# Performance work log

Hardware: AMD Instinct MI355X
Metric: run time of the kernel (lower is better)

## Reference

```python
import jax, jax.numpy as jnp
import numpy as np

B, C, IMG, P = 64, 3, 224, 16
D, L, H, DH, M, NC = 768, 12, 12, 64, 3072, 1000
INNER = H * DH
PD = C * P * P          # patch_dim = 768
NP = (IMG // P) ** 2    # 196 patches


def setup_inputs() -> dict:
    key = jax.random.key(0)
    ks = jax.random.split(key, 16)
    s = 0.02
    nrm = lambda k, shape: jax.random.normal(k, shape, jnp.float32) * s
    return dict(
        img=jax.random.normal(ks[0], (B, C, IMG, IMG), jnp.float32),
        patch_ln1_g=jnp.ones(PD), patch_ln1_b=jnp.zeros(PD),
        patch_w=nrm(ks[1], (PD, D)), patch_b=jnp.zeros(D),
        patch_ln2_g=jnp.ones(D), patch_ln2_b=jnp.zeros(D),
        pos_emb=nrm(ks[2], (1, NP + 1, D)),
        cls_tok=nrm(ks[3], (1, 1, D)),
        attn_ln_g=jnp.ones((L, D)), attn_ln_b=jnp.zeros((L, D)),
        w_qkv=nrm(ks[4], (L, D, 3 * INNER)),
        w_out=nrm(ks[5], (L, INNER, D)), b_out=jnp.zeros((L, D)),
        ff_ln_g=jnp.ones((L, D)), ff_ln_b=jnp.zeros((L, D)),
        ff_w1=nrm(ks[6], (L, D, M)), ff_b1=jnp.zeros((L, M)),
        ff_w2=nrm(ks[7], (L, M, D)), ff_b2=jnp.zeros((L, D)),
        final_ln_g=jnp.ones(D), final_ln_b=jnp.zeros(D),
        head_w=nrm(ks[8], (D, NC)), head_b=jnp.zeros(NC),
    )


def _ln(x, g, b, eps=1e-5):
    m = x.mean(-1, keepdims=True)
    v = ((x - m) ** 2).mean(-1, keepdims=True)
    return (x - m) / jnp.sqrt(v + eps) * g + b


def reference(img, patch_ln1_g, patch_ln1_b, patch_w, patch_b, patch_ln2_g,
              patch_ln2_b, pos_emb, cls_tok, attn_ln_g, attn_ln_b, w_qkv,
              w_out, b_out, ff_ln_g, ff_ln_b, ff_w1, ff_b1, ff_w2, ff_b2,
              final_ln_g, final_ln_b, head_w, head_b):
    b, c, hh, ww = img.shape
    h, w = hh // P, ww // P
    # Rearrange 'b c (h p1) (w p2) -> b (h w) (p1 p2 c)'
    x = img.reshape(b, c, h, P, w, P).transpose(0, 2, 4, 3, 5, 1).reshape(b, h * w, P * P * c)
    x = _ln(x, patch_ln1_g, patch_ln1_b)
    x = x @ patch_w + patch_b
    x = _ln(x, patch_ln2_g, patch_ln2_b)
    n = x.shape[1]
    x = jnp.concatenate([jnp.broadcast_to(cls_tok, (b, 1, x.shape[-1])), x], axis=1)
    x = x + pos_emb[:, : n + 1]
    scale = DH ** -0.5
    for l in range(L):
        xn = _ln(x, attn_ln_g[l], attn_ln_b[l])
        qkv = xn @ w_qkv[l]  # [b, n+1, 3*inner]
        q, k, v = jnp.split(qkv, 3, axis=-1)
        sp = lambda t: t.reshape(b, -1, H, DH).transpose(0, 2, 1, 3)  # b h n d
        q, k, v = sp(q), sp(k), sp(v)
        # softmax variant: exp(scores*scale), normalize by sum + eps (no max-subtract, faithful to source)
        numer = jnp.exp(jnp.einsum('bhid,bhjd->bhij', q, k) * scale)
        attn = numer / (numer.sum(-1, keepdims=True) + 1e-8)
        out = jnp.einsum('bhij,bhjd->bhid', attn, v)
        out = out.transpose(0, 2, 1, 3).reshape(b, -1, INNER)
        x = out @ w_out[l] + b_out[l] + x
        xn = _ln(x, ff_ln_g[l], ff_ln_b[l])
        hid = jax.nn.gelu(xn @ ff_w1[l] + ff_b1[l], approximate=False)
        x = hid @ ff_w2[l] + ff_b2[l] + x
    x = _ln(x, final_ln_g, final_ln_b)
    return x[:, 0] @ head_w + head_b
```

## Files before the change

### kernel.cpp

```cpp
#include <hip/hip_runtime.h>
#include <hip/hip_bf16.h>
#include <math.h>

#define B_     64
#define NTOK   197
#define NPATCH 196
#define D768   768
#define NL     12
#define NH     12
#define MFF    3072
#define NCLS   1000
#define ROWS   (B_ * NTOK)
#define PROWS  (B_ * NPATCH)
#define ROWS_PAD 12672

typedef unsigned short ushort;
typedef __bf16 bf16x8 __attribute__((ext_vector_type(8)));
typedef float  f32x4  __attribute__((ext_vector_type(4)));
typedef unsigned short u16x4 __attribute__((ext_vector_type(4)));

__device__ __forceinline__ ushort f2b(float f) {
  __hip_bfloat16 h = __float2bfloat16(f);
  return *reinterpret_cast<ushort*>(&h);
}
__device__ __forceinline__ float b2f(ushort u) {
  unsigned int v = ((unsigned int)u) << 16;
  float f;
  __builtin_memcpy(&f, &v, 4);
  return f;
}

__device__ __forceinline__ void gload16(const ushort* g, ushort* lds) {
  __builtin_amdgcn_global_load_lds((const __attribute__((address_space(1))) void*)g,
                                   (__attribute__((address_space(3))) void*)lds, 16, 0, 0);
}

__device__ __forceinline__ float gelu_f(float v) {
  float t = v * fmaf(0.0713548162726f, v * v, 1.5957691216f);
  return v / (1.0f + __expf(-t));
}

__device__ __forceinline__ void block_mean_rstd(float s, float sq, float& mean, float& rstd) {
#pragma unroll
  for (int off = 32; off; off >>= 1) { s += __shfl_xor(s, off); sq += __shfl_xor(sq, off); }
  __shared__ float ss[4], ssq[4];
  int w = threadIdx.x >> 6;
  if ((threadIdx.x & 63) == 0) { ss[w] = s; ssq[w] = sq; }
  __syncthreads();
  s  = ss[0] + ss[1] + ss[2] + ss[3];
  sq = ssq[0] + ssq[1] + ssq[2] + ssq[3];
  mean = s * (1.0f / 768.0f);
  float var = sq * (1.0f / 768.0f) - mean * mean;
  rstd = rsqrtf(var + 1e-5f);
}

__global__ __launch_bounds__(256) void ln_rows4(const ushort* __restrict__ in, long in_stride,
                                                const float* __restrict__ g,
                                                const float* __restrict__ bta,
                                                ushort* __restrict__ out) {
  const int w = threadIdx.x >> 6, l = threadIdx.x & 63;
  const size_t row = (size_t)blockIdx.x * 4 + w;
  const ushort* xr = in + row * in_stride;
  u16x4 xv[3];
  xv[0] = *(const u16x4*)(xr + l * 4);
  xv[1] = *(const u16x4*)(xr + 256 + l * 4);
  xv[2] = *(const u16x4*)(xr + 512 + l * 4);
  float v[12];
  float s = 0.f, sq = 0.f;
#pragma unroll
  for (int i = 0; i < 3; ++i)
#pragma unroll
    for (int j = 0; j < 4; ++j) {
      float f = b2f(xv[i][j]);
      v[i * 4 + j] = f;
      s += f; sq += f * f;
    }
#pragma unroll
  for (int off = 32; off; off >>= 1) { s += __shfl_xor(s, off); sq += __shfl_xor(sq, off); }
  float mean = s * (1.0f / 768.0f);
  float rstd = rsqrtf(sq * (1.0f / 768.0f) - mean * mean + 1e-5f);
  ushort* o = out + row * 768;
#pragma unroll
  for (int i = 0; i < 3; ++i) {
    int base = i * 256 + l * 4;
    f32x4 gv = *(const f32x4*)(g + base);
    f32x4 bv = *(const f32x4*)(bta + base);
    u16x4 ov = { f2b((v[i*4+0] - mean) * rstd * gv[0] + bv[0]),
                 f2b((v[i*4+1] - mean) * rstd * gv[1] + bv[1]),
                 f2b((v[i*4+2] - mean) * rstd * gv[2] + bv[2]),
                 f2b((v[i*4+3] - mean) * rstd * gv[3] + bv[3]) };
    *(u16x4*)(o + base) = ov;
  }
}

__global__ __launch_bounds__(256) void patch_ln1(const float* __restrict__ img,
                                                 const float* __restrict__ g,
                                                 const float* __restrict__ bta,
                                                 ushort* __restrict__ xp) {
  int pidx = blockIdx.x;
  int b = pidx / NPATCH, hw = pidx % NPATCH;
  int ph = hw / 14, pw = hw % 14;
  int t = threadIdx.x;
  int p1 = t >> 4, p2 = t & 15;
  float v[3];
#pragma unroll
  for (int c = 0; c < 3; ++c)
    v[c] = img[(((size_t)b * 3 + c) * 224 + ph * 16 + p1) * 224 + pw * 16 + p2];
  float mean, rstd;
  block_mean_rstd(v[0] + v[1] + v[2], v[0] * v[0] + v[1] * v[1] + v[2] * v[2], mean, rstd);
  ushort* o = xp + (size_t)pidx * 768;
#pragma unroll
  for (int c = 0; c < 3; ++c) {
    int k = t * 3 + c;
    o[k] = f2b((v[c] - mean) * rstd * g[k] + bta[k]);
  }
}

__global__ __launch_bounds__(256) void ln2_pos(const float* __restrict__ xe,
                                               const float* __restrict__ g,
                                               const float* __restrict__ bta,
                                               const float* __restrict__ pos,
                                               ushort* __restrict__ x) {
  int pidx = blockIdx.x;
  int b = pidx / NPATCH, i = pidx % NPATCH;
  const float* xr = xe + (size_t)pidx * 768;
  int t = threadIdx.x;
  float v0 = xr[t], v1 = xr[t + 256], v2 = xr[t + 512];
  float mean, rstd;
  block_mean_rstd(v0 + v1 + v2, v0 * v0 + v1 * v1 + v2 * v2, mean, rstd);
  const float* p = pos + (size_t)(1 + i) * 768;
  ushort* o = x + ((size_t)b * NTOK + 1 + i) * 768;
  o[t]       = f2b((v0 - mean) * rstd * g[t]       + bta[t]       + p[t]);
  o[t + 256] = f2b((v1 - mean) * rstd * g[t + 256] + bta[t + 256] + p[t + 256]);
  o[t + 512] = f2b((v2 - mean) * rstd * g[t + 512] + bta[t + 512] + p[t + 512]);
}

__global__ __launch_bounds__(256) void cls_init(const float* __restrict__ cls_tok,
                                                const float* __restrict__ pos,
                                                ushort* __restrict__ x) {
  int b = blockIdx.x, t = threadIdx.x;
  ushort* o = x + (size_t)b * NTOK * 768;
#pragma unroll
  for (int u = 0; u < 3; ++u) { int k = t + u * 256; o[k] = f2b(cls_tok[k] + pos[k]); }
}

__global__ __launch_bounds__(256) void transpose_cast(const float* __restrict__ W,
                                                      ushort* __restrict__ Wt,
                                                      int K, int N) {
  __shared__ float t[32][33];
  int n0 = blockIdx.x * 32, k0 = blockIdx.y * 32;
  int tx = threadIdx.x, ty = threadIdx.y;
#pragma unroll
  for (int u = 0; u < 32; u += 8) {
    int n = n0 + tx;
    t[ty + u][tx] = (n < N) ? W[(size_t)(k0 + ty + u) * N + n] : 0.f;
  }
  __syncthreads();
#pragma unroll
  for (int u = 0; u < 32; u += 8) {
    int n = n0 + ty + u;
    if (n < N) Wt[(size_t)n * K + k0 + tx] = f2b(t[tx][ty + u]);
  }
}

__device__ __forceinline__ void transpose_layer128(int bid,
                                                   const float* wq, const float* wo,
                                                   const float* w1, const float* w2,
                                                   ushort* tq, ushort* to,
                                                   ushort* t1, ushort* t2) {
  const float* W; ushort* Wt; int K, N, xt;
  if (bid < 216)      {             W = wq; Wt = tq; K = 768;  N = 2304; xt = 36; }
  else if (bid < 288) { bid -= 216; W = wo; Wt = to; K = 768;  N = 768;  xt = 12; }
  else if (bid < 576) { bid -= 288; W = w1; Wt = t1; K = 768;  N = 3072; xt = 48; }
  else                { bid -= 576; W = w2; Wt = t2; K = 3072; N = 768;  xt = 12; }
  int n0 = (bid % xt) * 64, k0 = (bid / xt) * 128;
  __shared__ float t[128 * 64];
  int id = threadIdx.x;
#pragma unroll
  for (int pass = 0; pass < 8; ++pass) {
    int c = pass * 256 + id;
    int k = c >> 4, col = (c & 15) * 4;
    f32x4 v = *(const f32x4*)(W + (size_t)(k0 + k) * N + n0 + col);
    int s = (k >> 2) & 31;
#pragma unroll
    for (int j = 0; j < 4; ++j) t[k * 64 + ((col + j) ^ s)] = v[j];
  }
  __syncthreads();
#pragma unroll
  for (int pass = 0; pass < 8; ++pass) {
    int c = pass * 256 + id;
    int n = c >> 5, k = (c & 31) * 4;
    int s = (k >> 2) & 31;
    u16x4 o = { f2b(t[(k + 0) * 64 + (n ^ s)]),
                f2b(t[(k + 1) * 64 + (n ^ s)]),
                f2b(t[(k + 2) * 64 + (n ^ s)]),
                f2b(t[(k + 3) * 64 + (n ^ s)]) };
    *(u16x4*)(Wt + (size_t)(n0 + n) * K + k0 + k) = o;
  }
}

__global__ __launch_bounds__(256) void transpose4(const float* __restrict__ wq,
                                                  const float* __restrict__ wo,
                                                  const float* __restrict__ w1,
                                                  const float* __restrict__ w2,
                                                  ushort* __restrict__ tq,
                                                  ushort* __restrict__ to,
                                                  ushort* __restrict__ t1,
                                                  ushort* __restrict__ t2) {
  transpose_layer128(blockIdx.x, wq, wo, w1, w2, tq, to, t1, t2);
}

__global__ __launch_bounds__(256) void transpose_all(const float* __restrict__ wq,
                                                     const float* __restrict__ wo,
                                                     const float* __restrict__ w1,
                                                     const float* __restrict__ w2,
                                                     ushort* __restrict__ tq,
                                                     ushort* __restrict__ to,
                                                     ushort* __restrict__ t1,
                                                     ushort* __restrict__ t2) {
  int l = blockIdx.x / 864, bid = blockIdx.x % 864;
  transpose_layer128(bid,
                     wq + (size_t)l * 768 * 2304, wo + (size_t)l * 768 * 768,
                     w1 + (size_t)l * 768 * MFF,  w2 + (size_t)l * MFF * 768,
                     tq + (size_t)l * 2304 * 768, to + (size_t)l * 768 * 768,
                     t1 + (size_t)l * MFF * 768,  t2 + (size_t)l * 768 * MFF);
}

template<int EP, int RESID, int OBF>
__global__ __launch_bounds__(256, 4) void gemm_v6(const ushort* __restrict__ A,
                                                  const ushort* __restrict__ Bt,
                                                  const float* __restrict__ bias,
                                                  const void* __restrict__ resid,
                                                  void* __restrict__ Cv,
                                                  int M, int N, int K) {
  __shared__ ushort smem[2 * 8192];

  const int tid = threadIdx.x;
  const int w = tid >> 6, l = tid & 63;
  const int fr = l & 15, fc = l >> 4;

  const int ntx = gridDim.x;
  const int nwg = ntx * gridDim.y;
  const int orig = blockIdx.y * ntx + blockIdx.x;
  const int q = nwg >> 3, r = nwg & 7, xcd = orig & 7, idx = orig >> 3;
  const int wg = (xcd < r ? xcd * (q + 1) : r * (q + 1) + (xcd - r) * q) + idx;
  const int row0 = (wg / ntx) * 128, col0 = (wg % ntx) * 128;

  const int wr = (w >> 1) * 64, wc = (w & 1) * 64;

  const int srow = tid >> 2;
  const int sg = (tid & 3) ^ ((srow >> 1) & 3);
  const ushort* pA0 = A  + (size_t)(row0 + srow) * K + sg * 8;
  const ushort* pA1 = A  + (size_t)(row0 + 64 + srow) * K + sg * 8;
  const ushort* pB0 = Bt + (size_t)(col0 + srow) * K + sg * 8;
  const ushort* pB1 = Bt + (size_t)(col0 + 64 + srow) * K + sg * 8;

  auto stage = [&](int t_, ushort* dst) {
    const int k0 = t_ * 32;
    gload16(pA0 + k0, dst + tid * 8);
    gload16(pA1 + k0, dst + (tid + 256) * 8);
    gload16(pB0 + k0, dst + 4096 + tid * 8);
    gload16(pB1 + k0, dst + 4096 + (tid + 256) * 8);
  };

  int idxA[4], idxB[4];
#pragma unroll
  for (int m = 0; m < 4; ++m) {
    int rA = wr + m * 16 + fr;
    idxA[m] = rA * 32 + ((fc ^ ((rA >> 1) & 3)) << 3);
  }
#pragma unroll
  for (int n = 0; n < 4; ++n) {
    int rB = wc + n * 16 + fr;
    idxB[n] = rB * 32 + ((fc ^ ((rB >> 1) & 3)) << 3);
  }

  f32x4 acc[4][4] = {};

  auto compute = [&](const ushort* As) {
    const ushort* Bs = As + 4096;
    bf16x8 a_[4], b_[4];
#pragma unroll
    for (int m = 0; m < 4; ++m) a_[m] = *(const bf16x8*)(As + idxA[m]);
#pragma unroll
    for (int n = 0; n < 4; ++n) b_[n] = *(const bf16x8*)(Bs + idxB[n]);
#pragma unroll
    for (int m = 0; m < 4; ++m)
#pragma unroll
      for (int n = 0; n < 4; ++n)
        acc[m][n] = __builtin_amdgcn_mfma_f32_16x16x32_bf16(b_[n], a_[m], acc[m][n], 0, 0, 0);
  };

#define VM4() asm volatile("s_waitcnt vmcnt(4)" ::: "memory")
#define VM0() asm volatile("s_waitcnt vmcnt(0)" ::: "memory")

  const int NT = K >> 5;

  stage(0, smem);
  for (int t = 0; t < NT; t += 2) {
    if (t + 1 < NT) { stage(t + 1, smem + 8192); VM4(); } else VM0();
    __builtin_amdgcn_s_barrier();
    compute(smem);
    __builtin_amdgcn_s_barrier();
    if (t + 1 < NT) {
      if (t + 2 < NT) { stage(t + 2, smem); VM4(); } else VM0();
      __builtin_amdgcn_s_barrier();
      compute(smem + 8192);
      __builtin_amdgcn_s_barrier();
    }
  }
#undef VM4
#undef VM0

  if (!OBF) {
    float* Cf = (float*)Cv;
#pragma unroll
    for (int m = 0; m < 4; ++m) {
      int row = row0 + wr + m * 16 + fr;
      if (row >= M) continue;
#pragma unroll
      for (int n = 0; n < 4; ++n) {
        int col = col0 + wc + n * 16 + fc * 4;
        f32x4 v = acc[m][n];
        if (bias) v += *(const f32x4*)(bias + col);
        if (EP) {
#pragma unroll
          for (int rr = 0; rr < 4; ++rr) v[rr] = gelu_f(v[rr]);
        }
        if (RESID) v += *(const f32x4*)((const float*)resid + (size_t)row * N + col);
        *(f32x4*)(Cf + (size_t)row * N + col) = v;
      }
    }
  } else {
    __syncthreads();
    ushort* Cw = smem + w * 4096;
#pragma unroll
    for (int m = 0; m < 4; ++m) {
      int rl = m * 16 + fr;
      int row = row0 + wr + rl;
#pragma unroll
      for (int n = 0; n < 4; ++n) {
        int col = col0 + wc + n * 16 + fc * 4;
        f32x4 v = acc[m][n];
        if (bias) v += *(const f32x4*)(bias + col);
        if (EP) {
#pragma unroll
          for (int rr = 0; rr < 4; ++rr) v[rr] = gelu_f(v[rr]);
        }
        if (RESID) {
          u16x4 rv = *(const u16x4*)((const ushort*)resid + (size_t)row * N + col);
#pragma unroll
          for (int rr = 0; rr < 4; ++rr) v[rr] += b2f(rv[rr]);
        }
        u16x4 pk = { f2b(v[0]), f2b(v[1]), f2b(v[2]), f2b(v[3]) };
        int s = (n * 4 + fc) ^ (rl & 7);
        *(u16x4*)(Cw + rl * 64 + s * 4) = pk;
      }
    }
    ushort* Cb = (ushort*)Cv;
#pragma unroll
    for (int pp = 0; pp < 16; ++pp) {
      int rl = pp * 4 + (l >> 4);
      int cs = l & 15;
      u16x4 pk = *(const u16x4*)(Cw + rl * 64 + ((cs ^ (rl & 7)) * 4));
      int row = row0 + wr + rl;
      if (row < M) *(u16x4*)(Cb + (size_t)row * N + col0 + wc + cs * 4) = pk;
    }
  }
}

template<int EP, int RESID, int OBF>
__global__ __launch_bounds__(256) void gemm_bt(const ushort* __restrict__ A,
                                               const ushort* __restrict__ Bt,
                                               const float* __restrict__ bias,
                                               const float* __restrict__ resid,
                                               void* __restrict__ C,
                                               int M, int N, int K) {
  __shared__ ushort As[128 * 32];
  __shared__ ushort Bs[128 * 32];
  int tid = threadIdx.x;
  int w = tid >> 6, l = tid & 63;
  int fr = l & 15, fc = l >> 4;
  int row0 = blockIdx.y * 128, col0 = blockIdx.x * 128;
  int wr = (w >> 1) * 64, wc = (w & 1) * 64;

  int srow0 = w * 32 + (l >> 2);
  int srow1 = srow0 + 16;
  int sc0 = (((l & 3) ^ ((srow0 >> 1) & 3)) << 3);
  int sc1 = (((l & 3) ^ ((srow1 >> 1) & 3)) << 3);
  const ushort* ga0 = A  + (size_t)(row0 + srow0) * K + sc0;
  const ushort* ga1 = A  + (size_t)(row0 + srow1) * K + sc1;
  const ushort* gb0 = Bt + (size_t)(col0 + srow0) * K + sc0;
  const ushort* gb1 = Bt + (size_t)(col0 + srow1) * K + sc1;

  int idxA[4], idxB[4];
#pragma unroll
  for (int m = 0; m < 4; ++m) {
    int rA = wr + m * 16 + fr;
    idxA[m] = rA * 32 + ((fc ^ ((rA >> 1) & 3)) << 3);
  }
#pragma unroll
  for (int n = 0; n < 4; ++n) {
    int rB = wc + n * 16 + fr;
    idxB[n] = rB * 32 + ((fc ^ ((rB >> 1) & 3)) << 3);
  }

  f32x4 acc[4][4] = {};

  for (int k0 = 0; k0 < K; k0 += 32) {
    gload16(ga0 + k0, &As[w * 1024]);
    gload16(ga1 + k0, &As[w * 1024 + 512]);
    gload16(gb0 + k0, &Bs[w * 1024]);
    gload16(gb1 + k0, &Bs[w * 1024 + 512]);
    __syncthreads();
    bf16x8 af[4], bfr[4];
#pragma unroll
    for (int m = 0; m < 4; ++m) af[m] = *(const bf16x8*)(As + idxA[m]);
#pragma unroll
    for (int n = 0; n < 4; ++n) bfr[n] = *(const bf16x8*)(Bs + idxB[n]);
#pragma unroll
    for (int m = 0; m < 4; ++m)
#pragma unroll
      for (int n = 0; n < 4; ++n)
        acc[m][n] = __builtin_amdgcn_mfma_f32_16x16x32_bf16(af[m], bfr[n], acc[m][n], 0, 0, 0);
    __syncthreads();
  }

#pragma unroll
  for (int n = 0; n < 4; ++n) {
    int col = col0 + wc + n * 16 + fr;
    if (col >= N) continue;
    float bv = bias ? bias[col] : 0.f;
#pragma unroll
    for (int m = 0; m < 4; ++m) {
#pragma unroll
      for (int rr = 0; rr < 4; ++rr) {
        int row = row0 + wr + m * 16 + fc * 4 + rr;
        if (row >= M) continue;
        float v = acc[m][n][rr] + bv;
        if (EP == 1) v = 0.5f * v * (1.0f + erff(v * 0.70710678118654752f));
        if (RESID) v += resid[(size_t)row * N + col];
        if (OBF) ((ushort*)C)[(size_t)row * N + col] = f2b(v);
        else     ((float*)C)[(size_t)row * N + col]  = v;
      }
    }
  }
}

__global__ __launch_bounds__(256) void attn_mfma(const ushort* __restrict__ qkv,
                                                 ushort* __restrict__ aout) {
  int bidp = blockIdx.x;
  int bh = (bidp & 7) | ((bidp >> 5) << 3);
  int qt = (bidp >> 3) & 3;
  int h  = bh % NH;
  int b  = bh / NH;
  int tid = threadIdx.x, w = tid >> 6, l = tid & 63;
  int fr = l & 15, fc = l >> 4;

  __shared__ ushort Kt[64 * 64];
  __shared__ ushort Vt[64 * 64];
  __shared__ ushort Pl[4 * 16 * 64];

  const size_t brow = (size_t)b * NTOK;
  int q0 = qt * 64 + w * 16;

  const int skey = tid >> 3;
  const int sgk = (tid & 7) ^ ((skey >> 1) & 7);
  const ushort* pK0 = qkv + (brow + skey) * 2304 + 768 + h * 64 + sgk * 8;
  const ushort* pK1 = qkv + (brow + 32 + skey) * 2304 + 768 + h * 64 + sgk * 8;

  bf16x8 qf[2];
  {
    const ushort* qp = qkv + (brow + q0 + fr) * 2304 + h * 64 + fc * 8;
    qf[0] = *(const bf16x8*)qp;
    qf[1] = *(const bf16x8*)(qp + 32);
  }
  float rs[4] = {0.f, 0.f, 0.f, 0.f};
  f32x4 oc[4] = {};

  for (int kt = 0; kt < 4; ++kt) {
    __syncthreads();
    {
      const size_t koff = (size_t)kt * 64 * 2304;
      gload16(pK0 + koff, Kt + tid * 8);
      gload16(pK1 + koff, Kt + (tid + 256) * 8);
    }
    {
      int key = tid >> 2, d0 = (tid & 3) * 16;
      int j = kt * 64 + key;
      bool valid = j < NTOK;
      const ushort* vp = qkv + (brow + j) * 2304 + 1536 + h * 64 + d0;
      ushort vbuf[16];
      if (valid) {
        *(bf16x8*)(vbuf)     = *(const bf16x8*)vp;
        *(bf16x8*)(vbuf + 8) = *(const bf16x8*)(vp + 8);
      } else {
#pragma unroll
        for (int i = 0; i < 16; ++i) vbuf[i] = 0;
      }
#pragma unroll
      for (int i = 0; i < 16; ++i) {
        int d = d0 + i;
        int byte = d * 128 + ((((key >> 3)) ^ (d & 7)) << 4) + (key & 7) * 2;
        Vt[byte >> 1] = vbuf[i];
      }
    }
    asm volatile("s_waitcnt vmcnt(0)" ::: "memory");
    __syncthreads();
    f32x4 sc[4];
#pragma unroll
    for (int n = 0; n < 4; ++n) {
      int row = n * 16 + fr;
      int sw = (row >> 1) & 7;
      const ushort* kr = Kt + row * 64;
      bf16x8 k0 = *(const bf16x8*)(kr + ((fc ^ sw) << 3));
      bf16x8 k1 = *(const bf16x8*)(kr + (((fc + 4) ^ sw) << 3));
      f32x4 z = {};
      z = __builtin_amdgcn_mfma_f32_16x16x32_bf16(qf[0], k0, z, 0, 0, 0);
      z = __builtin_amdgcn_mfma_f32_16x16x32_bf16(qf[1], k1, z, 0, 0, 0);
      sc[n] = z;
    }
    float part[4] = {0.f, 0.f, 0.f, 0.f};
#pragma unroll
    for (int n = 0; n < 4; ++n) {
      int j = kt * 64 + n * 16 + fr;
      bool jv = j < NTOK;
#pragma unroll
      for (int rr = 0; rr < 4; ++rr) {
        float e = jv ? __expf(sc[n][rr] * 0.125f) : 0.f;
        part[rr] += e;
        int row = fc * 4 + rr, col = n * 16 + fr;
        int byte = row * 128 + (((col >> 3) ^ (row & 7)) << 4) + (col & 7) * 2;
        Pl[w * 1024 + (byte >> 1)] = f2b(e);
      }
    }
#pragma unroll
    for (int rr = 0; rr < 4; ++rr) {
      float p = part[rr];
      p += __shfl_xor(p, 1); p += __shfl_xor(p, 2);
      p += __shfl_xor(p, 4); p += __shfl_xor(p, 8);
      rs[rr] += p;
    }
    __syncthreads();
#pragma unroll
    for (int ks = 0; ks < 2; ++ks) {
      int prow = fr;
      int pbyte = prow * 128 + (((ks * 4 + fc) ^ (prow & 7)) << 4);
      bf16x8 pf = *(const bf16x8*)(Pl + w * 1024 + (pbyte >> 1));
#pragma unroll
      for (int n = 0; n < 4; ++n) {
        int d = n * 16 + fr;
        int vb = d * 128 + (((ks * 4 + fc) ^ (d & 7)) << 4);
        bf16x8 vf = *(const bf16x8*)(Vt + (vb >> 1));
        oc[n] = __builtin_amdgcn_mfma_f32_16x16x32_bf16(pf, vf, oc[n], 0, 0, 0);
      }
    }
  }
  __syncthreads();
  ushort* Ow = Pl + w * 1024;
#pragma unroll
  for (int n = 0; n < 4; ++n)
#pragma unroll
    for (int rr = 0; rr < 4; ++rr) {
      float v = oc[n][rr] / (rs[rr] + 1e-8f);
      Ow[(fc * 4 + rr) * 64 + n * 16 + fr] = f2b(v);
    }
  asm volatile("s_waitcnt lgkmcnt(0)" ::: "memory");
#pragma unroll
  for (int pass = 0; pass < 4; ++pass) {
    int rl = pass * 4 + (l >> 4);
    int d0 = (l & 15) * 4;
    u16x4 pk = *(const u16x4*)(Ow + rl * 64 + d0);
    int qq = q0 + rl;
    if (qq < NTOK)
      *(u16x4*)(aout + (brow + qq) * 768 + h * 64 + d0) = pk;
  }
}

extern "C" void kernel_launch(void* const* d_in, const int* in_sizes, int n_in,
                              void* d_out, int out_size, void* d_ws, size_t ws_size,
                              hipStream_t stream) {
  const float* img       = (const float*)d_in[0];
  const float* p_ln1_g   = (const float*)d_in[1];
  const float* p_ln1_b   = (const float*)d_in[2];
  const float* patch_w   = (const float*)d_in[3];
  const float* patch_b   = (const float*)d_in[4];
  const float* p_ln2_g   = (const float*)d_in[5];
  const float* p_ln2_b   = (const float*)d_in[6];
  const float* pos_emb   = (const float*)d_in[7];
  const float* cls_tok   = (const float*)d_in[8];
  const float* attn_ln_g = (const float*)d_in[9];
  const float* attn_ln_b = (const float*)d_in[10];
  const float* w_qkv     = (const float*)d_in[11];
  const float* w_out     = (const float*)d_in[12];
  const float* b_out     = (const float*)d_in[13];
  const float* ff_ln_g   = (const float*)d_in[14];
  const float* ff_ln_b   = (const float*)d_in[15];
  const float* ff_w1     = (const float*)d_in[16];
  const float* ff_b1     = (const float*)d_in[17];
  const float* ff_w2     = (const float*)d_in[18];
  const float* ff_b2     = (const float*)d_in[19];
  const float* fin_ln_g  = (const float*)d_in[20];
  const float* fin_ln_b  = (const float*)d_in[21];
  const float* head_w    = (const float*)d_in[22];
  const float* head_b    = (const float*)d_in[23];
  float* out = (float*)d_out;

  char* p = (char*)d_ws;
  auto alloc = [&](size_t bytes) { char* r = p; p += (bytes + 255) & ~(size_t)255; return r; };
  ushort* x      = (ushort*)alloc((size_t)ROWS_PAD * 768 * 2);
  ushort* xnb    = (ushort*)alloc((size_t)ROWS_PAD * 768 * 2);
  ushort* qkvb   = (ushort*)alloc((size_t)ROWS_PAD * 2304 * 2);
  ushort* aoutb  = (ushort*)alloc((size_t)ROWS_PAD * 768 * 2);
  ushort* pwt    = (ushort*)alloc((size_t)768 * 768 * 2);
  ushort* hwt    = (ushort*)alloc((size_t)1024 * 768 * 2);
  ushort* xclsb  = (ushort*)alloc((size_t)128 * 768 * 2);
  ushort* hidb   = qkvb;
  ushort* xpb    = xnb;
  float*  xe     = (float*)qkvb;

  const size_t SQ = (size_t)2304 * 768, SO = (size_t)768 * 768, S1 = (size_t)MFF * 768;
  size_t used = (size_t)(p - (char*)d_ws);
  bool oneshot = (used + 12 * (SQ + SO + 2 * S1) * 2 + 4096) <= ws_size;
  int nw = oneshot ? 12 : 1;
  ushort* wtq = (ushort*)alloc(nw * SQ * 2);
  ushort* wto = (ushort*)alloc(nw * SO * 2);
  ushort* wt1 = (ushort*)alloc(nw * S1 * 2);
  ushort* wt2 = (ushort*)alloc(nw * S1 * 2);

  dim3 blk(256), tblk(32, 8);

  transpose_cast<<<dim3(24, 24), tblk, 0, stream>>>(patch_w, pwt, 768, 768);
  transpose_cast<<<dim3(32, 24), tblk, 0, stream>>>(head_w, hwt, 768, 1000);
  if (oneshot)
    transpose_all<<<12 * 864, blk, 0, stream>>>(w_qkv, w_out, ff_w1, ff_w2,
                                                wtq, wto, wt1, wt2);
  patch_ln1<<<PROWS, blk, 0, stream>>>(img, p_ln1_g, p_ln1_b, xpb);
  gemm_v6<0, 0, 0><<<dim3(6, 98), blk, 0, stream>>>(xpb, pwt, patch_b, nullptr, xe,
                                                    PROWS, 768, 768);
  ln2_pos<<<PROWS, blk, 0, stream>>>(xe, p_ln2_g, p_ln2_b, pos_emb, x);
  cls_init<<<B_, blk, 0, stream>>>(cls_tok, pos_emb, x);

  for (int l = 0; l < NL; ++l) {
    ushort* tq = wtq + (oneshot ? (size_t)l * SQ : 0);
    ushort* to = wto + (oneshot ? (size_t)l * SO : 0);
    ushort* t1 = wt1 + (oneshot ? (size_t)l * S1 : 0);
    ushort* t2 = wt2 + (oneshot ? (size_t)l * S1 : 0);
    if (!oneshot)
      transpose4<<<864, blk, 0, stream>>>(w_qkv + (size_t)l * 768 * 2304,
                                          w_out + (size_t)l * 768 * 768,
                                          ff_w1 + (size_t)l * 768 * MFF,
                                          ff_w2 + (size_t)l * MFF * 768,
                                          tq, to, t1, t2);

    ln_rows4<<<ROWS / 4, blk, 0, stream>>>(x, 768, attn_ln_g + (size_t)l * 768,
                                           attn_ln_b + (size_t)l * 768, xnb);
    gemm_v6<0, 0, 1><<<dim3(18, 99), blk, 0, stream>>>(xnb, tq, nullptr, nullptr, qkvb,
                                                       ROWS, 2304, 768);
    attn_mfma<<<B_ * NH * 4, blk, 0, stream>>>(qkvb, aoutb);
    gemm_v6<0, 1, 1><<<dim3(6, 99), blk, 0, stream>>>(aoutb, to, b_out + (size_t)l * 768,
                                                      x, x, ROWS, 768, 768);
    ln_rows4<<<ROWS / 4, blk, 0, stream>>>(x, 768, ff_ln_g + (size_t)l * 768,
                                           ff_ln_b + (size_t)l * 768, xnb);
    gemm_v6<1, 0, 1><<<dim3(24, 99), blk, 0, stream>>>(xnb, t1, ff_b1 + (size_t)l * MFF,
                                                       nullptr, hidb, ROWS, MFF, 768);
    gemm_v6<0, 1, 1><<<dim3(6, 99), blk, 0, stream>>>(hidb, t2, ff_b2 + (size_t)l * 768,
                                                      x, x, ROWS, 768, MFF);
  }

  ln_rows4<<<B_ / 4, blk, 0, stream>>>(x, (long)NTOK * 768, fin_ln_g, fin_ln_b, xclsb);
  gemm_bt<0, 0, 0><<<dim3(8, 1), blk, 0, stream>>>(xclsb, hwt, head_b, nullptr, out,
                                                   B_, NCLS, 768);
}
```

Before: 4.036 ms.

## Process all query tiles per block to reuse K/V loads in attention

The attention kernel now launches one block per (batch, head) instead of four, and each wave loops over all four query tiles. K and V tiles are staged into shared memory once and reused across the query tiles, which removes redundant global loads. The per-wave P buffer is reused across query tiles, with lgkmcnt waits replacing a block barrier. In exchange, block count drops fourfold (768 blocks), register pressure rises from holding 4x accumulators and Q fragments, and the qt loop is not unrolled.

```diff
diff --git a/kernel.cpp b/kernel.cpp
--- a/kernel.cpp
+++ b/kernel.cpp
@@ -447,11 +447,9 @@
   }
 }
 
-__global__ __launch_bounds__(256) void attn_mfma(const ushort* __restrict__ qkv,
-                                                 ushort* __restrict__ aout) {
-  int bidp = blockIdx.x;
-  int bh = (bidp & 7) | ((bidp >> 5) << 3);
-  int qt = (bidp >> 3) & 3;
+__global__ __launch_bounds__(256) void attn_mfma2(const ushort* __restrict__ qkv,
+                                                  ushort* __restrict__ aout) {
+  int bh = blockIdx.x;
   int h  = bh % NH;
   int b  = bh / NH;
   int tid = threadIdx.x, w = tid >> 6, l = tid & 63;
@@ -462,21 +460,21 @@
   __shared__ ushort Pl[4 * 16 * 64];
 
   const size_t brow = (size_t)b * NTOK;
-  int q0 = qt * 64 + w * 16;
 
   const int skey = tid >> 3;
   const int sgk = (tid & 7) ^ ((skey >> 1) & 7);
   const ushort* pK0 = qkv + (brow + skey) * 2304 + 768 + h * 64 + sgk * 8;
   const ushort* pK1 = qkv + (brow + 32 + skey) * 2304 + 768 + h * 64 + sgk * 8;
 
-  bf16x8 qf[2];
-  {
-    const ushort* qp = qkv + (brow + q0 + fr) * 2304 + h * 64 + fc * 8;
-    qf[0] = *(const bf16x8*)qp;
-    qf[1] = *(const bf16x8*)(qp + 32);
-  }
-  float rs[4] = {0.f, 0.f, 0.f, 0.f};
-  f32x4 oc[4] = {};
+  bf16x8 qf[4][2];
+#pragma unroll
+  for (int qt = 0; qt < 4; ++qt) {
+    const ushort* qp = qkv + (brow + qt * 64 + w * 16 + fr) * 2304 + h * 64 + fc * 8;
+    qf[qt][0] = *(const bf16x8*)qp;
+    qf[qt][1] = *(const bf16x8*)(qp + 32);
+  }
+  float rs[4][4] = {};
+  f32x4 oc[4][4] = {};
 
   for (int kt = 0; kt < 4; ++kt) {
     __syncthreads();
@@ -507,73 +505,79 @@
     }
     asm volatile("s_waitcnt vmcnt(0)" ::: "memory");
     __syncthreads();
-    f32x4 sc[4];
-#pragma unroll
-    for (int n = 0; n < 4; ++n) {
-      int row = n * 16 + fr;
-      int sw = (row >> 1) & 7;
-      const ushort* kr = Kt + row * 64;
-      bf16x8 k0 = *(const bf16x8*)(kr + ((fc ^ sw) << 3));
-      bf16x8 k1 = *(const bf16x8*)(kr + (((fc + 4) ^ sw) << 3));
-      f32x4 z = {};
-      z = __builtin_amdgcn_mfma_f32_16x16x32_bf16(qf[0], k0, z, 0, 0, 0);
-      z = __builtin_amdgcn_mfma_f32_16x16x32_bf16(qf[1], k1, z, 0, 0, 0);
-      sc[n] = z;
-    }
-    float part[4] = {0.f, 0.f, 0.f, 0.f};
-#pragma unroll
-    for (int n = 0; n < 4; ++n) {
-      int j = kt * 64 + n * 16 + fr;
-      bool jv = j < NTOK;
+
+    for (int qt = 0; qt < 4; ++qt) {
+      f32x4 sc[4];
+#pragma unroll
+      for (int n = 0; n < 4; ++n) {
+        int row = n * 16 + fr;
+        int sw = (row >> 1) & 7;
+        const ushort* kr = Kt + row * 64;
+        bf16x8 k0 = *(const bf16x8*)(kr + ((fc ^ sw) << 3));
+        bf16x8 k1 = *(const bf16x8*)(kr + (((fc + 4) ^ sw) << 3));
+        f32x4 z = {};
+        z = __builtin_amdgcn_mfma_f32_16x16x32_bf16(qf[qt][0], k0, z, 0, 0, 0);
+        z = __builtin_amdgcn_mfma_f32_16x16x32_bf16(qf[qt][1], k1, z, 0, 0, 0);
+        sc[n] = z;
+      }
+      float part[4] = {0.f, 0.f, 0.f, 0.f};
+#pragma unroll
+      for (int n = 0; n < 4; ++n) {
+        int j = kt * 64 + n * 16 + fr;
+        bool jv = j < NTOK;
+#pragma unroll
+        for (int rr = 0; rr < 4; ++rr) {
+          float e = jv ? __expf(sc[n][rr] * 0.125f) : 0.f;
+          part[rr] += e;
+          int row = fc * 4 + rr, col = n * 16 + fr;
+          int byte = row * 128 + (((col >> 3) ^ (row & 7)) << 4) + (col & 7) * 2;
+          Pl[w * 1024 + (byte >> 1)] = f2b(e);
+        }
+      }
 #pragma unroll
       for (int rr = 0; rr < 4; ++rr) {
-        float e = jv ? __expf(sc[n][rr] * 0.125f) : 0.f;
-        part[rr] += e;
-        int row = fc * 4 + rr, col = n * 16 + fr;
-        int byte = row * 128 + (((col >> 3) ^ (row & 7)) << 4) + (col & 7) * 2;
-        Pl[w * 1024 + (byte >> 1)] = f2b(e);
-      }
-    }
-#pragma unroll
-    for (int rr = 0; rr < 4; ++rr) {
-      float p = part[rr];
-      p += __shfl_xor(p, 1); p += __shfl_xor(p, 2);
-      p += __shfl_xor(p, 4); p += __shfl_xor(p, 8);
-      rs[rr] += p;
-    }
-    __syncthreads();
-#pragma unroll
-    for (int ks = 0; ks < 2; ++ks) {
-      int prow = fr;
-      int pbyte = prow * 128 + (((ks * 4 + fc) ^ (prow & 7)) << 4);
-      bf16x8 pf = *(const bf16x8*)(Pl + w * 1024 + (pbyte >> 1));
-#pragma unroll
-      for (int n = 0; n < 4; ++n) {
-        int d = n * 16 + fr;
-        int vb = d * 128 + (((ks * 4 + fc) ^ (d & 7)) << 4);
-        bf16x8 vf = *(const bf16x8*)(Vt + (vb >> 1));
-        oc[n] = __builtin_amdgcn_mfma_f32_16x16x32_bf16(pf, vf, oc[n], 0, 0, 0);
+        float p = part[rr];
+        p += __shfl_xor(p, 1); p += __shfl_xor(p, 2);
+        p += __shfl_xor(p, 4); p += __shfl_xor(p, 8);
+        rs[qt][rr] += p;
+      }
+      asm volatile("s_waitcnt lgkmcnt(0)" ::: "memory");
+#pragma unroll
+      for (int ks = 0; ks < 2; ++ks) {
+        int prow = fr;
+        int pbyte = prow * 128 + (((ks * 4 + fc) ^ (prow & 7)) << 4);
+        bf16x8 pf = *(const bf16x8*)(Pl + w * 1024 + (pbyte >> 1));
+#pragma unroll
+        for (int n = 0; n < 4; ++n) {
+          int d = n * 16 + fr;
+          int vb = d * 128 + (((ks * 4 + fc) ^ (d & 7)) << 4);
+          bf16x8 vf = *(const bf16x8*)(Vt + (vb >> 1));
+          oc[qt][n] = __builtin_amdgcn_mfma_f32_16x16x32_bf16(pf, vf, oc[qt][n], 0, 0, 0);
+        }
       }
     }
   }
   __syncthreads();
   ushort* Ow = Pl + w * 1024;
-#pragma unroll
-  for (int n = 0; n < 4; ++n)
-#pragma unroll
-    for (int rr = 0; rr < 4; ++rr) {
-      float v = oc[n][rr] / (rs[rr] + 1e-8f);
-      Ow[(fc * 4 + rr) * 64 + n * 16 + fr] = f2b(v);
-    }
-  asm volatile("s_waitcnt lgkmcnt(0)" ::: "memory");
-#pragma unroll
-  for (int pass = 0; pass < 4; ++pass) {
-    int rl = pass * 4 + (l >> 4);
-    int d0 = (l & 15) * 4;
-    u16x4 pk = *(const u16x4*)(Ow + rl * 64 + d0);
-    int qq = q0 + rl;
-    if (qq < NTOK)
-      *(u16x4*)(aout + (brow + qq) * 768 + h * 64 + d0) = pk;
+  for (int qt = 0; qt < 4; ++qt) {
+#pragma unroll
+    for (int n = 0; n < 4; ++n)
+#pragma unroll
+      for (int rr = 0; rr < 4; ++rr) {
+        float v = oc[qt][n][rr] / (rs[qt][rr] + 1e-8f);
+        Ow[(fc * 4 + rr) * 64 + n * 16 + fr] = f2b(v);
+      }
+    asm volatile("s_waitcnt lgkmcnt(0)" ::: "memory");
+#pragma unroll
+    for (int pass = 0; pass < 4; ++pass) {
+      int rl = pass * 4 + (l >> 4);
+      int d0 = (l & 15) * 4;
+      u16x4 pk = *(const u16x4*)(Ow + rl * 64 + d0);
+      int qq = qt * 64 + w * 16 + rl;
+      if (qq < NTOK)
+        *(u16x4*)(aout + (brow + qq) * 768 + h * 64 + d0) = pk;
+    }
+    asm volatile("s_waitcnt lgkmcnt(0)" ::: "memory");
   }
 }
 
@@ -657,7 +661,7 @@
                                            attn_ln_b + (size_t)l * 768, xnb);
     gemm_v6<0, 0, 1><<<dim3(18, 99), blk, 0, stream>>>(xnb, tq, nullptr, nullptr, qkvb,
                                                        ROWS, 2304, 768);
-    attn_mfma<<<B_ * NH * 4, blk, 0, stream>>>(qkvb, aoutb);
+    attn_mfma2<<<B_ * NH, blk, 0, stream>>>(qkvb, aoutb);
     gemm_v6<0, 1, 1><<<dim3(6, 99), blk, 0, stream>>>(aoutb, to, b_out + (size_t)l * 768,
                                                       x, x, ROWS, 768, 768);
     ln_rows4<<<ROWS / 4, blk, 0, stream>>>(x, 768, ff_ln_g + (size_t)l * 768,
```

New measurement: 4.059 ms. No clear change (+0.6%).
